# Performance work log

Measured on AMD Instinct MI355X. Metric: run time of the kernel, lower is better.

## Reference

```python
import jax, jax.numpy as jnp
import numpy as np

NEG = -1e15  # matches mask_logits constant -1000000000000000.0


def setup_inputs() -> dict:
    key = jax.random.key(0)
    ks = jax.random.split(key, 4)
    B, d, c_len, q_len = 64, 512, 1024, 128
    C = jax.random.normal(ks[0], (B, d, c_len), dtype=jnp.float32)
    Q = jax.random.normal(ks[1], (B, d, q_len), dtype=jnp.float32)
    c_mask = jnp.ones((B, c_len), dtype=jnp.float32)
    q_mask = jnp.ones((B, q_len), dtype=jnp.float32)
    W0 = jax.random.normal(ks[2], (3 * d,), dtype=jnp.float32) / np.sqrt(d).astype(np.float32)
    Wr = jax.random.normal(ks[3], (d, 4 * d), dtype=jnp.float32) * np.float32(0.02)
    return {"C": C, "Q": Q, "c_mask": c_mask, "q_mask": q_mask, "W0": W0, "Wr": Wr}


def reference(C, Q, c_mask, q_mask, W0, Wr):
    # C: [B, d, c], Q: [B, d, q]
    d = C.shape[1]
    C_t = jnp.swapaxes(C, 1, 2)  # [B, c, d]
    Q_t = jnp.swapaxes(Q, 1, 2)  # [B, q, d]
    w_c, w_q, w_m = W0[:d], W0[d:2 * d], W0[2 * d:]
    # Trilinear similarity, algebraically identical to cat([C,Q,C*Q]) @ W0
    S = (C_t @ w_c)[:, :, None] + (Q_t @ w_q)[:, None, :] \
        + jnp.einsum('bid,bjd->bij', C_t * w_m, Q_t)  # [B, c, q]
    qm = q_mask[:, None, :]  # [B, 1, q]
    cm = c_mask[:, :, None]  # [B, c, 1]
    S_bar = jax.nn.softmax(S * qm + NEG * (1.0 - qm), axis=2)
    S_bbar = jax.nn.softmax(S * cm + NEG * (1.0 - cm), axis=1)
    A = S_bar @ Q_t  # [B, c, d]
    Bm = jnp.einsum('bij,bkj->bik', S_bar, S_bbar) @ C_t  # [B, c, d]
    out = jnp.concatenate([C_t, A, C_t * A, C_t * Bm], axis=2)  # [B, c, 4d]
    # dropout inactive (eval mode); 1x1 conv == matmul with Wr [d, 4d]
    return jnp.einsum('od,bcd->boc', Wr, out)  # [B, d, c]
```

## Files before the change

kernel.cpp:

```cpp
#include <hip/hip_runtime.h>
#include <hip/hip_bf16.h>

typedef unsigned short u16;
typedef __attribute__((ext_vector_type(8))) short short8;
typedef __attribute__((ext_vector_type(4))) short short4v;
typedef __attribute__((ext_vector_type(4))) float f32x4;

#define NEGV -1000000000000000.0f
#define SBAR() asm volatile("s_barrier" ::: "memory")

__device__ __forceinline__ u16 f2bf(float f) {
  unsigned u = __float_as_uint(f);
  unsigned r = (u + 0x7FFFu + ((u >> 16) & 1u)) >> 16;
  return (u16)r;
}
__device__ __forceinline__ float bf2f(u16 s) {
  return __uint_as_float(((unsigned)s) << 16);
}
__device__ __forceinline__ void lds16(const void* g, void* l) {
  __builtin_amdgcn_global_load_lds((const __attribute__((address_space(1))) void*)g,
                                   (__attribute__((address_space(3))) void*)l,
                                   16, 0, 0);
}

__global__ __launch_bounds__(1024) void gemm8b(const u16* __restrict__ A,
                                               const u16* __restrict__ B,
                                               float* __restrict__ out) {
  extern __shared__ u16 lds[];
  const int bid = blockIdx.x;
  const int wg = (bid & 7) * 64 + (bid >> 3);
  const int m0 = (wg & 1) * 256;
  const int n0 = (wg >> 1) * 256;
  const int tid = threadIdx.x;
  const int lane = tid & 63;
  const int w = tid >> 6;
  const int wr = w >> 2;
  const int wc = w & 3;
  const int fro = lane & 15;
  const int hi = lane >> 4;
  const int kx = fro & 7;
  const int sr = lane >> 3;
  const int sgc = ((lane & 7) ^ sr) << 3;

  const u16* Ag = A + (size_t)m0 * 2048;
  const u16* Bg = B + (size_t)n0 * 2048;
  const int rA = wr * 64 + fro;
  const int rB = wc * 64 + fro;

  f32x4 acc[4][4] = {};

#define STG(gp, lp) \
  lds16((gp) + (size_t)(w * 8 + sr) * 2048 + sgc, (u16*)(lp) + w * 512)
#define RDF(base, row, k16) \
  (*(const short8*)&(base)[(size_t)(row) * 64 + (((k16) ^ kx) << 3)])

  STG(Ag, lds);
  STG(Ag + 262144, lds + 8192);
  STG(Bg, lds + 32768);
  STG(Bg + 262144, lds + 32768 + 8192);
  STG(Bg + 64, lds + 49152);
  STG(Bg + 262144 + 64, lds + 49152 + 8192);
  asm volatile("s_waitcnt vmcnt(2)" ::: "memory");
  SBAR();

  const u16* Ac = lds;
  u16* An = lds + 16384;
  const u16* Bc = lds + 32768;
  const u16* Bn = lds + 49152;
  u16* Bs2 = lds + 65536;

  for (int t = 0; t < 32; ++t) {
    const int kkA = (t < 31 ? t + 1 : 31) * 64;
    const int kkB = (t < 30 ? t + 2 : 31) * 64;
    short8 af[4], bf[4];

#pragma unroll
    for (int i = 0; i < 4; ++i) af[i] = RDF(Ac, rA + i * 16, hi);
#pragma unroll
    for (int j = 0; j < 4; ++j) bf[j] = RDF(Bc, rB + j * 16, hi);
    STG(Ag + kkA, An);
    STG(Ag + 262144 + kkA, An + 8192);
    SBAR();
    __builtin_amdgcn_s_setprio(1);
#pragma unroll
    for (int i = 0; i < 4; ++i)
#pragma unroll
      for (int j = 0; j < 4; ++j)
        acc[i][j] =
            __builtin_amdgcn_mfma_f32_16x16x32_bf16(af[i], bf[j], acc[i][j], 0, 0, 0);
    __builtin_amdgcn_s_setprio(0);
    SBAR();

#pragma unroll
    for (int i = 0; i < 4; ++i) af[i] = RDF(Ac, rA + i * 16, 4 + hi);
#pragma unroll
    for (int j = 0; j < 4; ++j) bf[j] = RDF(Bc, rB + j * 16, 4 + hi);
    STG(Bg + kkB, Bs2);
    STG(Bg + 262144 + kkB, Bs2 + 8192);
    asm volatile("s_waitcnt vmcnt(2)" ::: "memory");
    SBAR();
    __builtin_amdgcn_s_setprio(1);
#pragma unroll
    for (int i = 0; i < 4; ++i)
#pragma unroll
      for (int j = 0; j < 4; ++j)
        acc[i][j] =
            __builtin_amdgcn_mfma_f32_16x16x32_bf16(af[i], bf[j], acc[i][j], 0, 0, 0);
    __builtin_amdgcn_s_setprio(0);
    SBAR();

    u16* tA = An; An = (u16*)Ac; Ac = tA;
    u16* tB = (u16*)Bc; Bc = Bn; Bn = Bs2; Bs2 = tB;
  }
  asm volatile("s_waitcnt vmcnt(0)" ::: "memory");

  const int crow = m0 + wr * 64 + hi * 4;
#pragma unroll
  for (int i = 0; i < 4; ++i)
#pragma unroll
    for (int j = 0; j < 4; ++j) {
      const int n = n0 + wc * 64 + j * 16 + fro;
      float* op = out + (size_t)(n >> 10) * 524288 + (n & 1023);
#pragma unroll
      for (int g = 0; g < 4; ++g)
        op[(size_t)(crow + i * 16 + g) * 1024] = acc[i][j][g];
    }
#undef STG
#undef RDF
}

__global__ __launch_bounds__(256) void gemm_t(const u16* __restrict__ A,
                                              const u16* __restrict__ B,
                                              const float* __restrict__ csum,
                                              u16* __restrict__ Tt) {
  __shared__ u16 As[128 * 64];
  __shared__ u16 Bs[128 * 64];
  const int b = blockIdx.z;
  const int n0 = blockIdx.y * 128;
  const u16* Ab = A + (size_t)b * 131072;
  const u16* Bb = B + (size_t)b * 524288;
  const int t = threadIdx.x;
  const int lane = t & 63;
  const int w = t >> 6;
  const int wr = w >> 1, wc = w & 1;
  const int srow = lane >> 3;
  const int scol = (lane & 7) * 8;

  f32x4 acc[4][4] = {};

  for (int k0 = 0; k0 < 1024; k0 += 64) {
    __syncthreads();
#pragma unroll
    for (int qq = 0; qq < 4; ++qq) {
      const int q = w * 4 + qq;
      const int r = q * 8 + srow;
      lds16(Ab + (size_t)r * 1024 + k0 + scol, &As[q * 512]);
      lds16(Bb + (size_t)(n0 + r) * 1024 + k0 + scol, &Bs[q * 512]);
    }
    __syncthreads();
#pragma unroll
    for (int ks = 0; ks < 2; ++ks) {
      short8 af[4], bg[4];
      const int fro = lane & 15;
      const int k8 = ks * 32 + (lane >> 4) * 8;
#pragma unroll
      for (int i = 0; i < 4; ++i)
        af[i] = *(const short8*)&As[(wr * 64 + i * 16 + fro) * 64 + k8];
#pragma unroll
      for (int i = 0; i < 4; ++i)
        bg[i] = *(const short8*)&Bs[(wc * 64 + i * 16 + fro) * 64 + k8];
#pragma unroll
      for (int i = 0; i < 4; ++i)
#pragma unroll
        for (int j = 0; j < 4; ++j)
          acc[i][j] =
              __builtin_amdgcn_mfma_f32_16x16x32_bf16(af[i], bg[j], acc[i][j], 0, 0, 0);
    }
  }

  const int col = lane & 15;
  const int r4 = (lane >> 4) * 4;
#pragma unroll
  for (int i = 0; i < 4; ++i)
#pragma unroll
    for (int g = 0; g < 4; ++g) {
      const int rr = wr * 64 + i * 16 + r4 + g;
      const float inv = 1.f / csum[b * 128 + rr];
#pragma unroll
      for (int j = 0; j < 4; ++j) {
        const int cc = n0 + wc * 64 + j * 16 + col;
        Tt[(size_t)b * 65536 + (size_t)cc * 128 + rr] = f2bf(acc[i][j][g] * inv);
      }
    }
}

__global__ __launch_bounds__(256) void gemm_s(
    const u16* __restrict__ A, const u16* __restrict__ Bq,
    const float* __restrict__ cb, const float* __restrict__ qb,
    const float* __restrict__ cmask, const float* __restrict__ qmask,
    u16* __restrict__ Sbar, u16* __restrict__ EunT, float* __restrict__ csum) {
  __shared__ u16 As[128 * 64];
  __shared__ u16 Bs[128 * 64];
  __shared__ u16 Lt[128][136];
  __shared__ float rmaxs[2][128];
  __shared__ float rsums[2][128];
  __shared__ float cparts[2][128];
  const int b = blockIdx.z;
  const int m0 = blockIdx.x * 128;
  const u16* Ab = A + (size_t)b * 2097152;
  const u16* Bb = Bq + (size_t)b * 65536;
  const int t = threadIdx.x;
  const int lane = t & 63;
  const int w = t >> 6;
  const int wr = w >> 1, wc = w & 1;
  const int srow = lane >> 3;
  const int scol = (lane & 7) * 8;

  f32x4 acc[4][4] = {};

  for (int k0 = 0; k0 < 512; k0 += 64) {
    __syncthreads();
#pragma unroll
    for (int qq = 0; qq < 4; ++qq) {
      const int q = w * 4 + qq;
      const int r = q * 8 + srow;
      lds16(Ab + (size_t)(m0 + r) * 2048 + k0 + scol, &As[q * 512]);
      lds16(Bb + (size_t)r * 512 + k0 + scol, &Bs[q * 512]);
    }
    __syncthreads();
#pragma unroll
    for (int ks = 0; ks < 2; ++ks) {
      short8 af[4], bg[4];
      const int fro = lane & 15;
      const int k8 = ks * 32 + (lane >> 4) * 8;
#pragma unroll
      for (int i = 0; i < 4; ++i)
        af[i] = *(const short8*)&As[(wr * 64 + i * 16 + fro) * 64 + k8];
#pragma unroll
      for (int i = 0; i < 4; ++i)
        bg[i] = *(const short8*)&Bs[(wc * 64 + i * 16 + fro) * 64 + k8];
#pragma unroll
      for (int i = 0; i < 4; ++i)
#pragma unroll
        for (int j = 0; j < 4; ++j)
          acc[i][j] =
              __builtin_amdgcn_mfma_f32_16x16x32_bf16(af[i], bg[j], acc[i][j], 0, 0, 0);
    }
  }

  const int fro = lane & 15;
  const int hi = lane >> 4;
  float qv[4], qbv[4];
#pragma unroll
  for (int j = 0; j < 4; ++j) {
    const int cc = wc * 64 + j * 16 + fro;
    qv[j] = qmask[b * 128 + cc];
    qbv[j] = qb[b * 128 + cc];
  }
  float colp[4] = {0.f, 0.f, 0.f, 0.f};
#pragma unroll
  for (int i = 0; i < 4; ++i)
#pragma unroll
    for (int g = 0; g < 4; ++g) {
      const int rl = wr * 64 + i * 16 + hi * 4 + g;
      const float rb = cb[b * 1024 + m0 + rl];
      const float cv = cmask[b * 1024 + m0 + rl];
      const float coff = NEGV * (1.f - cv);
#pragma unroll
      for (int j = 0; j < 4; ++j) {
        const float v = acc[i][j][g] + rb + qbv[j];
        acc[i][j][g] = v;
        const float e = __expf(v * cv + coff);
        Lt[wc * 64 + j * 16 + fro][rl] = f2bf(e);
        colp[j] += e;
      }
    }
#pragma unroll
  for (int j = 0; j < 4; ++j) {
    colp[j] += __shfl_xor(colp[j], 16);
    colp[j] += __shfl_xor(colp[j], 32);
  }
  if (hi == 0)
#pragma unroll
    for (int j = 0; j < 4; ++j) cparts[wr][wc * 64 + j * 16 + fro] = colp[j];
  float rtmp[4][4];
#pragma unroll
  for (int i = 0; i < 4; ++i)
#pragma unroll
    for (int g = 0; g < 4; ++g) {
      float m = -3.4e38f;
#pragma unroll
      for (int j = 0; j < 4; ++j) {
        const float xm = acc[i][j][g] * qv[j] + NEGV * (1.f - qv[j]);
        acc[i][j][g] = xm;
        m = fmaxf(m, xm);
      }
#pragma unroll
      for (int o = 8; o; o >>= 1) m = fmaxf(m, __shfl_xor(m, o));
      rtmp[i][g] = m;
    }
  if (fro == 0)
#pragma unroll
    for (int i = 0; i < 4; ++i)
#pragma unroll
      for (int g = 0; g < 4; ++g)
        rmaxs[wc][wr * 64 + i * 16 + hi * 4 + g] = rtmp[i][g];
  __syncthreads();
  if (t < 128) atomicAdd(&csum[b * 128 + t], cparts[0][t] + cparts[1][t]);
  {
    const int jr = t >> 1;
    const int ih = (t & 1) * 64;
    u16* dst = EunT + (size_t)b * 131072 + (size_t)jr * 1024 + m0 + ih;
#pragma unroll
    for (int s = 0; s < 8; ++s)
      *(short8*)(dst + s * 8) = *(const short8*)&Lt[jr][ih + s * 8];
  }
#pragma unroll
  for (int i = 0; i < 4; ++i)
#pragma unroll
    for (int g = 0; g < 4; ++g) {
      const int rl = wr * 64 + i * 16 + hi * 4 + g;
      const float M = fmaxf(rmaxs[0][rl], rmaxs[1][rl]);
      float s = 0.f;
#pragma unroll
      for (int j = 0; j < 4; ++j) {
        const float p = __expf(acc[i][j][g] - M);
        acc[i][j][g] = p;
        s += p;
      }
#pragma unroll
      for (int o = 8; o; o >>= 1) s += __shfl_xor(s, o);
      rtmp[i][g] = s;
    }
  if (fro == 0)
#pragma unroll
    for (int i = 0; i < 4; ++i)
#pragma unroll
      for (int g = 0; g < 4; ++g)
        rsums[wc][wr * 64 + i * 16 + hi * 4 + g] = rtmp[i][g];
  __syncthreads();
#pragma unroll
  for (int i = 0; i < 4; ++i)
#pragma unroll
    for (int g = 0; g < 4; ++g) {
      const int rl = wr * 64 + i * 16 + hi * 4 + g;
      const float inv = 1.f / (rsums[0][rl] + rsums[1][rl]);
#pragma unroll
      for (int j = 0; j < 4; ++j)
        Sbar[((size_t)b * 1024 + m0 + rl) * 128 + wc * 64 + j * 16 + fro] =
            f2bf(acc[i][j][g] * inv);
    }
}

__global__ __launch_bounds__(512) void gemm_ab2(const u16* __restrict__ Sbar,
                                                const u16* __restrict__ Qo,
                                                const u16* __restrict__ Tt,
                                                u16* __restrict__ O) {
  extern __shared__ u16 sh[];
  u16* LQ = sh;
  u16* LT = sh + 16384;
  u16* Ls = sh + 65536;
  const int dcol = blockIdx.x * 128;
  const int b = blockIdx.y;
  const int t = threadIdx.x;
  const int lane = t & 63;
  const int w = t >> 6;
  const int wr = w >> 2, wc = w & 3;
  const int fro = lane & 15, hi = lane >> 4;
  const int srow4 = t >> 4;
  const int sslot = t & 15;

  const u16* Qg = Qo + (size_t)b * 65536 + (size_t)dcol * 128;
  const u16* Tg = Tt + (size_t)b * 65536 + (size_t)dcol * 128;
  const u16* Sg = Sbar + (size_t)b * 131072;

#define STG32(gp, lp)                                                         \
  {                                                                           \
    _Pragma("unroll") for (int ii = 0; ii < 4; ++ii) {                        \
      const int row_ = ii * 32 + srow4;                                       \
      lds16((gp) + (size_t)row_ * 128 + ((sslot ^ (row_ & 7)) << 3),          \
            (u16*)(lp) + ii * 4096 + t * 8);                                  \
    }                                                                         \
  }
#define RDS(base, row, kslot)                                                 \
  (*(const short8*)&(base)[(size_t)(row) * 128 + (((kslot) ^ ((row) & 7)) << 3)])

  STG32(Qg, LQ);
  STG32(Tg, LT);
  STG32(Sg, sh + 32768);
  asm volatile("s_waitcnt vmcnt(0)" ::: "memory");
  __syncthreads();

  for (int mm = 0; mm < 8; ++mm) {
    const u16* LSc = sh + 32768 + ((size_t)(mm & 1) << 14);
    u16* LSn = sh + 32768 + ((size_t)((mm + 1) & 1) << 14);
    if (mm < 7) STG32(Sg + (size_t)(mm + 1) * 16384, LSn);

    f32x4 aa[4][2] = {};
    f32x4 ab[4][2] = {};
#pragma unroll
    for (int ks = 0; ks < 4; ++ks) {
      short8 af[4], bq[2], bt[2];
#pragma unroll
      for (int i = 0; i < 4; ++i) {
        const int r = wr * 64 + i * 16 + fro;
        af[i] = RDS(LSc, r, ks * 4 + hi);
      }
#pragma unroll
      for (int j = 0; j < 2; ++j) {
        const int r = wc * 32 + j * 16 + fro;
        bq[j] = RDS(LQ, r, ks * 4 + hi);
        bt[j] = RDS(LT, r, ks * 4 + hi);
      }
#pragma unroll
      for (int i = 0; i < 4; ++i)
#pragma unroll
        for (int j = 0; j < 2; ++j) {
          aa[i][j] =
              __builtin_amdgcn_mfma_f32_16x16x32_bf16(af[i], bq[j], aa[i][j], 0, 0, 0);
          ab[i][j] =
              __builtin_amdgcn_mfma_f32_16x16x32_bf16(af[i], bt[j], ab[i][j], 0, 0, 0);
        }
    }

    const size_t obase = (size_t)b * 2097152 + (size_t)mm * 262144 + dcol;
    __syncthreads();
#pragma unroll
    for (int i = 0; i < 4; ++i)
#pragma unroll
      for (int j = 0; j < 2; ++j)
#pragma unroll
        for (int g = 0; g < 4; ++g)
          Ls[(wr * 64 + i * 16 + hi * 4 + g) * 128 + wc * 32 + j * 16 + fro] =
              f2bf(aa[i][j][g]);
    __syncthreads();
    short8 c8[4];
#pragma unroll
    for (int it = 0; it < 4; ++it) {
      const int row = it * 32 + srow4;
      const short8 a8 = *(const short8*)&Ls[row * 128 + sslot * 8];
      c8[it] = *(const short8*)&O[obase + (size_t)row * 2048 + sslot * 8];
      short8 p2;
#pragma unroll
      for (int k = 0; k < 8; ++k)
        p2[k] = (short)f2bf(bf2f((u16)c8[it][k]) * bf2f((u16)a8[k]));
      *(short8*)&O[obase + (size_t)row * 2048 + sslot * 8 + 512] = a8;
      *(short8*)&O[obase + (size_t)row * 2048 + sslot * 8 + 1024] = p2;
    }
    __syncthreads();
#pragma unroll
    for (int i = 0; i < 4; ++i)
#pragma unroll
      for (int j = 0; j < 2; ++j)
#pragma unroll
        for (int g = 0; g < 4; ++g)
          Ls[(wr * 64 + i * 16 + hi * 4 + g) * 128 + wc * 32 + j * 16 + fro] =
              f2bf(ab[i][j][g]);
    __syncthreads();
#pragma unroll
    for (int it = 0; it < 4; ++it) {
      const int row = it * 32 + srow4;
      const short8 b8 = *(const short8*)&Ls[row * 128 + sslot * 8];
      short8 p3;
#pragma unroll
      for (int k = 0; k < 8; ++k)
        p3[k] = (short)f2bf(bf2f((u16)c8[it][k]) * bf2f((u16)b8[k]));
      *(short8*)&O[obase + (size_t)row * 2048 + sslot * 8 + 1536] = p3;
    }
    __syncthreads();
  }
#undef STG32
#undef RDS
}

__global__ __launch_bounds__(256) void prep_C(const float* __restrict__ C,
                                              const float* __restrict__ W0,
                                              u16* __restrict__ O,
                                              u16* __restrict__ Corig,
                                              float* __restrict__ cb) {
  __shared__ float L[64][65];
  __shared__ float P[4][64];
  const int b = blockIdx.z;
  const int d0 = blockIdx.y * 64;
  const int i0 = blockIdx.x * 64;
  const int t = threadIdx.x;
  const int cx = t & 63;
  const int rb = t >> 6;
  const float* Cb = C + ((size_t)b * 512 + d0) * 1024 + i0;
  float part = 0.f;
#pragma unroll
  for (int rr = 0; rr < 16; ++rr) {
    const int r = rb * 16 + rr;
    const float v = Cb[(size_t)r * 1024 + cx];
    L[r][cx] = v;
    part = fmaf(v, W0[d0 + r], part);
    Corig[((size_t)b * 512 + d0 + r) * 1024 + i0 + cx] = f2bf(v);
  }
  P[rb][cx] = part;
  __syncthreads();
#pragma unroll
  for (int rr = 0; rr < 16; ++rr) {
    const int il = rb * 16 + rr;
    O[((size_t)b * 1024 + i0 + il) * 2048 + d0 + cx] = f2bf(L[cx][il]);
  }
  if (rb == 0)
    atomicAdd(&cb[b * 1024 + i0 + cx], P[0][cx] + P[1][cx] + P[2][cx] + P[3][cx]);
}

__global__ __launch_bounds__(256) void prep_Q(const float* __restrict__ Q,
                                              const float* __restrict__ W0,
                                              u16* __restrict__ Qmb,
                                              u16* __restrict__ Qorig,
                                              float* __restrict__ qb) {
  __shared__ float L[64][65];
  __shared__ float P[4][64];
  const int b = blockIdx.z;
  const int d0 = blockIdx.y * 64;
  const int j0 = blockIdx.x * 64;
  const int t = threadIdx.x;
  const int cx = t & 63;
  const int rb = t >> 6;
  const float* Qb = Q + ((size_t)b * 512 + d0) * 128 + j0;
  float part = 0.f;
#pragma unroll
  for (int rr = 0; rr < 16; ++rr) {
    const int r = rb * 16 + rr;
    const float v = Qb[(size_t)r * 128 + cx];
    L[r][cx] = v;
    part = fmaf(v, W0[512 + d0 + r], part);
    Qorig[((size_t)b * 512 + d0 + r) * 128 + j0 + cx] = f2bf(v);
  }
  P[rb][cx] = part;
  __syncthreads();
  const float wm = W0[1024 + d0 + cx];
#pragma unroll
  for (int rr = 0; rr < 16; ++rr) {
    const int jl = rb * 16 + rr;
    Qmb[((size_t)b * 128 + j0 + jl) * 512 + d0 + cx] = f2bf(L[cx][jl] * wm);
  }
  if (rb == 0)
    atomicAdd(&qb[b * 128 + j0 + cx], P[0][cx] + P[1][cx] + P[2][cx] + P[3][cx]);
}

__global__ __launch_bounds__(256) void cvt_wr(const float* __restrict__ Wr,
                                              u16* __restrict__ Wrb) {
  const int idx = blockIdx.x * 256 + threadIdx.x;
  const float4 v = ((const float4*)Wr)[idx];
  short4v o;
  o[0] = (short)f2bf(v.x);
  o[1] = (short)f2bf(v.y);
  o[2] = (short)f2bf(v.z);
  o[3] = (short)f2bf(v.w);
  *(short4v*)&Wrb[(size_t)idx * 4] = o;
}

extern "C" void kernel_launch(void* const* d_in, const int* in_sizes, int n_in,
                              void* d_out, int out_size, void* d_ws, size_t ws_size,
                              hipStream_t stream) {
  (void)in_sizes; (void)n_in; (void)out_size;
  const float* C = (const float*)d_in[0];
  const float* Q = (const float*)d_in[1];
  const float* cm = (const float*)d_in[2];
  const float* qm = (const float*)d_in[3];
  const float* W0 = (const float*)d_in[4];
  const float* Wr = (const float*)d_in[5];
  float* out = (float*)d_out;

  if (ws_size < 405078016ull) return;

  char* p = (char*)d_ws;
  u16* O     = (u16*)(p);
  u16* Corig = (u16*)(p + 268435456ull);
  u16* Qmb   = (u16*)(p + 335544320ull);
  u16* Qorig = (u16*)(p + 343932928ull);
  u16* EunT  = (u16*)(p + 360710144ull);
  u16* Sbar  = (u16*)(p + 377487360ull);
  u16* Tt    = (u16*)(p + 394264576ull);
  u16* Wrb   = (u16*)(p + 402653184ull);
  float* cb  = (float*)(p + 404750336ull);
  float* qb  = (float*)(p + 405012480ull);
  float* csum= (float*)(p + 405045248ull);

  (void)hipFuncSetAttribute((const void*)gemm8b,
                            hipFuncAttributeMaxDynamicSharedMemorySize, 163840);
  (void)hipFuncSetAttribute((const void*)gemm_ab2,
                            hipFuncAttributeMaxDynamicSharedMemorySize, 163840);
  (void)hipMemsetAsync(cb, 0, 327680, stream);

  cvt_wr<<<dim3(1024), dim3(256), 0, stream>>>(Wr, Wrb);
  prep_C<<<dim3(16, 8, 64), dim3(256), 0, stream>>>(C, W0, O, Corig, cb);
  prep_Q<<<dim3(2, 8, 64), dim3(256), 0, stream>>>(Q, W0, Qmb, Qorig, qb);

  gemm_s<<<dim3(8, 1, 64), dim3(256), 0, stream>>>(O, Qmb, cb, qb, cm, qm,
                                                   Sbar, EunT, csum);

  gemm_t<<<dim3(1, 4, 64), dim3(256), 0, stream>>>(EunT, Corig, csum, Tt);

  gemm_ab2<<<dim3(4, 64), dim3(512), 163840, stream>>>(Sbar, Qorig, Tt, O);

  gemm8b<<<dim3(512), dim3(1024), 163840, stream>>>(Wrb, O, out);
}
```

Before: 355.7 us.

## Fuse attention-output GEMMs with final projection to drop the concat buffer

Replaces the separate gemm_ab2 and gemm8b kernels with one fused kernel, gemm_f. For each 128-row context tile it computes S_bar·Q, S_bar·T and the elementwise products with C in LDS, then multiplies each 128-wide chunk directly by the matching slice of Wr. This removes the large [B, c, 4d] bf16 intermediate, which was written to and read back from global memory. prep_C and gemm_s now use a compact 512-stride C^T buffer, and the workspace shrinks. The cost is that every block re-streams all of Wr through LDS with no double-buffering and many barriers, and the 160KB LDS footprint limits occupancy to one block per CU. The tuned pipelined projection GEMM is lost as well.

```diff
diff --git a/kernel.cpp b/kernel.cpp
--- a/kernel.cpp
+++ b/kernel.cpp
@@ -7,7 +7,6 @@
 typedef __attribute__((ext_vector_type(4))) float f32x4;
 
 #define NEGV -1000000000000000.0f
-#define SBAR() asm volatile("s_barrier" ::: "memory")
 
 __device__ __forceinline__ u16 f2bf(float f) {
   unsigned u = __float_as_uint(f);
@@ -23,110 +22,155 @@
                                    16, 0, 0);
 }
 
-__global__ __launch_bounds__(1024) void gemm8b(const u16* __restrict__ A,
-                                               const u16* __restrict__ B,
-                                               float* __restrict__ out) {
-  extern __shared__ u16 lds[];
-  const int bid = blockIdx.x;
-  const int wg = (bid & 7) * 64 + (bid >> 3);
-  const int m0 = (wg & 1) * 256;
-  const int n0 = (wg >> 1) * 256;
-  const int tid = threadIdx.x;
-  const int lane = tid & 63;
-  const int w = tid >> 6;
-  const int wr = w >> 2;
-  const int wc = w & 3;
-  const int fro = lane & 15;
-  const int hi = lane >> 4;
-  const int kx = fro & 7;
-  const int sr = lane >> 3;
-  const int sgc = ((lane & 7) ^ sr) << 3;
-
-  const u16* Ag = A + (size_t)m0 * 2048;
-  const u16* Bg = B + (size_t)n0 * 2048;
-  const int rA = wr * 64 + fro;
-  const int rB = wc * 64 + fro;
-
-  f32x4 acc[4][4] = {};
-
-#define STG(gp, lp) \
-  lds16((gp) + (size_t)(w * 8 + sr) * 2048 + sgc, (u16*)(lp) + w * 512)
-#define RDF(base, row, k16) \
-  (*(const short8*)&(base)[(size_t)(row) * 64 + (((k16) ^ kx) << 3)])
-
-  STG(Ag, lds);
-  STG(Ag + 262144, lds + 8192);
-  STG(Bg, lds + 32768);
-  STG(Bg + 262144, lds + 32768 + 8192);
-  STG(Bg + 64, lds + 49152);
-  STG(Bg + 262144 + 64, lds + 49152 + 8192);
-  asm volatile("s_waitcnt vmcnt(2)" ::: "memory");
-  SBAR();
-
-  const u16* Ac = lds;
-  u16* An = lds + 16384;
-  const u16* Bc = lds + 32768;
-  const u16* Bn = lds + 49152;
-  u16* Bs2 = lds + 65536;
-
-  for (int t = 0; t < 32; ++t) {
-    const int kkA = (t < 31 ? t + 1 : 31) * 64;
-    const int kkB = (t < 30 ? t + 2 : 31) * 64;
-    short8 af[4], bf[4];
-
-#pragma unroll
-    for (int i = 0; i < 4; ++i) af[i] = RDF(Ac, rA + i * 16, hi);
-#pragma unroll
-    for (int j = 0; j < 4; ++j) bf[j] = RDF(Bc, rB + j * 16, hi);
-    STG(Ag + kkA, An);
-    STG(Ag + 262144 + kkA, An + 8192);
-    SBAR();
-    __builtin_amdgcn_s_setprio(1);
+__global__ __launch_bounds__(512, 2) void gemm_f(
+    const u16* __restrict__ Sb, const u16* __restrict__ Qo,
+    const u16* __restrict__ Tt, const u16* __restrict__ Ct,
+    const u16* __restrict__ Wrb, float* __restrict__ out) {
+  extern __shared__ u16 sh[];
+  u16* S  = sh;
+  u16* R1 = sh + 16384;
+  u16* R2 = sh + 32768;
+  u16* R3 = sh + 49152;
+  u16* R4 = sh + 65536;
+  const int mt = blockIdx.x;
+  const int b  = blockIdx.y;
+  const int m0 = mt * 128;
+  const int t = threadIdx.x;
+  const int lane = t & 63;
+  const int w = t >> 6;
+  const int fro = lane & 15, hi = lane >> 4;
+  const int srow4 = t >> 4;
+  const int sslot = t & 15;
+  const int o1 = (w >> 1) * 64;
+  const int cb2 = (w & 1) * 64;
+
+#define STG32(gp, ld, lp)                                                     \
+  {                                                                           \
+    _Pragma("unroll") for (int ii = 0; ii < 4; ++ii) {                        \
+      const int row_ = ii * 32 + srow4;                                       \
+      lds16((gp) + (size_t)row_ * (ld) + ((sslot ^ (row_ & 7)) << 3),         \
+            (u16*)(lp) + ii * 4096 + t * 8);                                  \
+    }                                                                         \
+  }
+#define RDS(base, row, kslot)                                                 \
+  (*(const short8*)&(base)[(size_t)(row) * 128 + (((kslot) ^ ((row) & 7)) << 3)])
+
+  f32x4 OA[2][4][4] = {};
+
+  STG32(Sb + (size_t)b * 131072 + (size_t)m0 * 128, 128, S);
+  __syncthreads();
+
+  for (int dcol = 0; dcol < 4; ++dcol) {
+    STG32(Qo + (size_t)b * 65536 + (size_t)(dcol * 128) * 128, 128, R1);
+    STG32(Tt + (size_t)b * 65536 + (size_t)(dcol * 128) * 128, 128, R2);
+    STG32(Ct + (size_t)b * 524288 + (size_t)m0 * 512 + dcol * 128, 512, R4);
+    __syncthreads();
+
+    {
+      f32x4 p[8] = {};
+#pragma unroll
+      for (int ks = 0; ks < 4; ++ks) {
+        const short8 af = RDS(S, w * 16 + fro, ks * 4 + hi);
+        short8 bf[8];
+#pragma unroll
+        for (int jd = 0; jd < 8; ++jd) bf[jd] = RDS(R2, jd * 16 + fro, ks * 4 + hi);
+#pragma unroll
+        for (int jd = 0; jd < 8; ++jd)
+          p[jd] = __builtin_amdgcn_mfma_f32_16x16x32_bf16(af, bf[jd], p[jd], 0, 0, 0);
+      }
+#pragma unroll
+      for (int jd = 0; jd < 8; ++jd)
+#pragma unroll
+        for (int g = 0; g < 4; ++g) {
+          const int c = w * 16 + hi * 4 + g;
+          const int d = jd * 16 + fro;
+          const int a = c * 128 + (((d >> 3) ^ (c & 7)) << 3) + (d & 7);
+          R3[a] = f2bf(p[jd][g] * bf2f(R4[a]));
+        }
+    }
+    f32x4 paa[8] = {};
+#pragma unroll
+    for (int ks = 0; ks < 4; ++ks) {
+      const short8 af = RDS(S, w * 16 + fro, ks * 4 + hi);
+      short8 bf[8];
+#pragma unroll
+      for (int jd = 0; jd < 8; ++jd) bf[jd] = RDS(R1, jd * 16 + fro, ks * 4 + hi);
+#pragma unroll
+      for (int jd = 0; jd < 8; ++jd)
+        paa[jd] = __builtin_amdgcn_mfma_f32_16x16x32_bf16(af, bf[jd], paa[jd], 0, 0, 0);
+    }
+    __syncthreads();
+
+#pragma unroll
+    for (int cc = 0; cc < 4; ++cc) {
+      const int ch = (cc == 0) ? 3 : cc - 1;
+      if (ch == 1 || ch == 2) {
+#pragma unroll
+        for (int jd = 0; jd < 8; ++jd)
+#pragma unroll
+          for (int g = 0; g < 4; ++g) {
+            const int c = w * 16 + hi * 4 + g;
+            const int d = jd * 16 + fro;
+            const int a = c * 128 + (((d >> 3) ^ (c & 7)) << 3) + (d & 7);
+            R3[a] = f2bf(ch == 1 ? paa[jd][g] : paa[jd][g] * bf2f(R4[a]));
+          }
+      }
+      const u16* Wp = Wrb + (size_t)ch * 512 + (size_t)dcol * 128;
+      STG32(Wp, 2048, R1);
+      STG32(Wp + (size_t)128 * 2048, 2048, R2);
+      __syncthreads();
+      const u16* Bp = (ch == 0) ? R4 : R3;
+#pragma unroll
+      for (int ks = 0; ks < 4; ++ks) {
+        short8 af[4], bfr[4];
+#pragma unroll
+        for (int i = 0; i < 4; ++i) af[i] = RDS(R1, o1 + i * 16 + fro, ks * 4 + hi);
+#pragma unroll
+        for (int j = 0; j < 4; ++j) bfr[j] = RDS(Bp, cb2 + j * 16 + fro, ks * 4 + hi);
+#pragma unroll
+        for (int i = 0; i < 4; ++i)
+#pragma unroll
+          for (int j = 0; j < 4; ++j)
+            OA[0][i][j] = __builtin_amdgcn_mfma_f32_16x16x32_bf16(
+                af[i], bfr[j], OA[0][i][j], 0, 0, 0);
+      }
+      __syncthreads();
+      STG32(Wp + (size_t)256 * 2048, 2048, R1);
+      STG32(Wp + (size_t)384 * 2048, 2048, R2);
+      __syncthreads();
+#pragma unroll
+      for (int ks = 0; ks < 4; ++ks) {
+        short8 af[4], bfr[4];
+#pragma unroll
+        for (int i = 0; i < 4; ++i) af[i] = RDS(R1, o1 + i * 16 + fro, ks * 4 + hi);
+#pragma unroll
+        for (int j = 0; j < 4; ++j) bfr[j] = RDS(Bp, cb2 + j * 16 + fro, ks * 4 + hi);
+#pragma unroll
+        for (int i = 0; i < 4; ++i)
+#pragma unroll
+          for (int j = 0; j < 4; ++j)
+            OA[1][i][j] = __builtin_amdgcn_mfma_f32_16x16x32_bf16(
+                af[i], bfr[j], OA[1][i][j], 0, 0, 0);
+      }
+      __syncthreads();
+    }
+  }
+
+  float* ob = out + (size_t)b * 524288;
+#pragma unroll
+  for (int oh = 0; oh < 2; ++oh)
 #pragma unroll
     for (int i = 0; i < 4; ++i)
 #pragma unroll
-      for (int j = 0; j < 4; ++j)
-        acc[i][j] =
-            __builtin_amdgcn_mfma_f32_16x16x32_bf16(af[i], bf[j], acc[i][j], 0, 0, 0);
-    __builtin_amdgcn_s_setprio(0);
-    SBAR();
-
-#pragma unroll
-    for (int i = 0; i < 4; ++i) af[i] = RDF(Ac, rA + i * 16, 4 + hi);
-#pragma unroll
-    for (int j = 0; j < 4; ++j) bf[j] = RDF(Bc, rB + j * 16, 4 + hi);
-    STG(Bg + kkB, Bs2);
-    STG(Bg + 262144 + kkB, Bs2 + 8192);
-    asm volatile("s_waitcnt vmcnt(2)" ::: "memory");
-    SBAR();
-    __builtin_amdgcn_s_setprio(1);
-#pragma unroll
-    for (int i = 0; i < 4; ++i)
-#pragma unroll
-      for (int j = 0; j < 4; ++j)
-        acc[i][j] =
-            __builtin_amdgcn_mfma_f32_16x16x32_bf16(af[i], bf[j], acc[i][j], 0, 0, 0);
-    __builtin_amdgcn_s_setprio(0);
-    SBAR();
-
-    u16* tA = An; An = (u16*)Ac; Ac = tA;
-    u16* tB = (u16*)Bc; Bc = Bn; Bn = Bs2; Bs2 = tB;
-  }
-  asm volatile("s_waitcnt vmcnt(0)" ::: "memory");
-
-  const int crow = m0 + wr * 64 + hi * 4;
-#pragma unroll
-  for (int i = 0; i < 4; ++i)
-#pragma unroll
-    for (int j = 0; j < 4; ++j) {
-      const int n = n0 + wc * 64 + j * 16 + fro;
-      float* op = out + (size_t)(n >> 10) * 524288 + (n & 1023);
-#pragma unroll
-      for (int g = 0; g < 4; ++g)
-        op[(size_t)(crow + i * 16 + g) * 1024] = acc[i][j][g];
-    }
-#undef STG
-#undef RDF
+      for (int j = 0; j < 4; ++j) {
+        const int o = oh * 256 + o1 + i * 16 + hi * 4;
+        const int c = m0 + cb2 + j * 16 + fro;
+#pragma unroll
+        for (int g = 0; g < 4; ++g)
+          ob[(size_t)(o + g) * 1024 + c] = OA[oh][i][j][g];
+      }
+#undef STG32
+#undef RDS
 }
 
 __global__ __launch_bounds__(256) void gemm_t(const u16* __restrict__ A,
@@ -207,7 +251,7 @@
   __shared__ float cparts[2][128];
   const int b = blockIdx.z;
   const int m0 = blockIdx.x * 128;
-  const u16* Ab = A + (size_t)b * 2097152;
+  const u16* Ab = A + (size_t)b * 524288;
   const u16* Bb = Bq + (size_t)b * 65536;
   const int t = threadIdx.x;
   const int lane = t & 63;
@@ -224,7 +268,7 @@
     for (int qq = 0; qq < 4; ++qq) {
       const int q = w * 4 + qq;
       const int r = q * 8 + srow;
-      lds16(Ab + (size_t)(m0 + r) * 2048 + k0 + scol, &As[q * 512]);
+      lds16(Ab + (size_t)(m0 + r) * 512 + k0 + scol, &As[q * 512]);
       lds16(Bb + (size_t)r * 512 + k0 + scol, &Bs[q * 512]);
     }
     __syncthreads();
@@ -352,130 +396,9 @@
     }
 }
 
-__global__ __launch_bounds__(512) void gemm_ab2(const u16* __restrict__ Sbar,
-                                                const u16* __restrict__ Qo,
-                                                const u16* __restrict__ Tt,
-                                                u16* __restrict__ O) {
-  extern __shared__ u16 sh[];
-  u16* LQ = sh;
-  u16* LT = sh + 16384;
-  u16* Ls = sh + 65536;
-  const int dcol = blockIdx.x * 128;
-  const int b = blockIdx.y;
-  const int t = threadIdx.x;
-  const int lane = t & 63;
-  const int w = t >> 6;
-  const int wr = w >> 2, wc = w & 3;
-  const int fro = lane & 15, hi = lane >> 4;
-  const int srow4 = t >> 4;
-  const int sslot = t & 15;
-
-  const u16* Qg = Qo + (size_t)b * 65536 + (size_t)dcol * 128;
-  const u16* Tg = Tt + (size_t)b * 65536 + (size_t)dcol * 128;
-  const u16* Sg = Sbar + (size_t)b * 131072;
-
-#define STG32(gp, lp)                                                         \
-  {                                                                           \
-    _Pragma("unroll") for (int ii = 0; ii < 4; ++ii) {                        \
-      const int row_ = ii * 32 + srow4;                                       \
-      lds16((gp) + (size_t)row_ * 128 + ((sslot ^ (row_ & 7)) << 3),          \
-            (u16*)(lp) + ii * 4096 + t * 8);                                  \
-    }                                                                         \
-  }
-#define RDS(base, row, kslot)                                                 \
-  (*(const short8*)&(base)[(size_t)(row) * 128 + (((kslot) ^ ((row) & 7)) << 3)])
-
-  STG32(Qg, LQ);
-  STG32(Tg, LT);
-  STG32(Sg, sh + 32768);
-  asm volatile("s_waitcnt vmcnt(0)" ::: "memory");
-  __syncthreads();
-
-  for (int mm = 0; mm < 8; ++mm) {
-    const u16* LSc = sh + 32768 + ((size_t)(mm & 1) << 14);
-    u16* LSn = sh + 32768 + ((size_t)((mm + 1) & 1) << 14);
-    if (mm < 7) STG32(Sg + (size_t)(mm + 1) * 16384, LSn);
-
-    f32x4 aa[4][2] = {};
-    f32x4 ab[4][2] = {};
-#pragma unroll
-    for (int ks = 0; ks < 4; ++ks) {
-      short8 af[4], bq[2], bt[2];
-#pragma unroll
-      for (int i = 0; i < 4; ++i) {
-        const int r = wr * 64 + i * 16 + fro;
-        af[i] = RDS(LSc, r, ks * 4 + hi);
-      }
-#pragma unroll
-      for (int j = 0; j < 2; ++j) {
-        const int r = wc * 32 + j * 16 + fro;
-        bq[j] = RDS(LQ, r, ks * 4 + hi);
-        bt[j] = RDS(LT, r, ks * 4 + hi);
-      }
-#pragma unroll
-      for (int i = 0; i < 4; ++i)
-#pragma unroll
-        for (int j = 0; j < 2; ++j) {
-          aa[i][j] =
-              __builtin_amdgcn_mfma_f32_16x16x32_bf16(af[i], bq[j], aa[i][j], 0, 0, 0);
-          ab[i][j] =
-              __builtin_amdgcn_mfma_f32_16x16x32_bf16(af[i], bt[j], ab[i][j], 0, 0, 0);
-        }
-    }
-
-    const size_t obase = (size_t)b * 2097152 + (size_t)mm * 262144 + dcol;
-    __syncthreads();
-#pragma unroll
-    for (int i = 0; i < 4; ++i)
-#pragma unroll
-      for (int j = 0; j < 2; ++j)
-#pragma unroll
-        for (int g = 0; g < 4; ++g)
-          Ls[(wr * 64 + i * 16 + hi * 4 + g) * 128 + wc * 32 + j * 16 + fro] =
-              f2bf(aa[i][j][g]);
-    __syncthreads();
-    short8 c8[4];
-#pragma unroll
-    for (int it = 0; it < 4; ++it) {
-      const int row = it * 32 + srow4;
-      const short8 a8 = *(const short8*)&Ls[row * 128 + sslot * 8];
-      c8[it] = *(const short8*)&O[obase + (size_t)row * 2048 + sslot * 8];
-      short8 p2;
-#pragma unroll
-      for (int k = 0; k < 8; ++k)
-        p2[k] = (short)f2bf(bf2f((u16)c8[it][k]) * bf2f((u16)a8[k]));
-      *(short8*)&O[obase + (size_t)row * 2048 + sslot * 8 + 512] = a8;
-      *(short8*)&O[obase + (size_t)row * 2048 + sslot * 8 + 1024] = p2;
-    }
-    __syncthreads();
-#pragma unroll
-    for (int i = 0; i < 4; ++i)
-#pragma unroll
-      for (int j = 0; j < 2; ++j)
-#pragma unroll
-        for (int g = 0; g < 4; ++g)
-          Ls[(wr * 64 + i * 16 + hi * 4 + g) * 128 + wc * 32 + j * 16 + fro] =
-              f2bf(ab[i][j][g]);
-    __syncthreads();
-#pragma unroll
-    for (int it = 0; it < 4; ++it) {
-      const int row = it * 32 + srow4;
-      const short8 b8 = *(const short8*)&Ls[row * 128 + sslot * 8];
-      short8 p3;
-#pragma unroll
-      for (int k = 0; k < 8; ++k)
-        p3[k] = (short)f2bf(bf2f((u16)c8[it][k]) * bf2f((u16)b8[k]));
-      *(short8*)&O[obase + (size_t)row * 2048 + sslot * 8 + 1536] = p3;
-    }
-    __syncthreads();
-  }
-#undef STG32
-#undef RDS
-}
-
 __global__ __launch_bounds__(256) void prep_C(const float* __restrict__ C,
                                               const float* __restrict__ W0,
-                                              u16* __restrict__ O,
+                                              u16* __restrict__ Ct,
                                               u16* __restrict__ Corig,
                                               float* __restrict__ cb) {
   __shared__ float L[64][65];
@@ -501,7 +424,7 @@
 #pragma unroll
   for (int rr = 0; rr < 16; ++rr) {
     const int il = rb * 16 + rr;
-    O[((size_t)b * 1024 + i0 + il) * 2048 + d0 + cx] = f2bf(L[cx][il]);
+    Ct[((size_t)b * 1024 + i0 + il) * 512 + d0 + cx] = f2bf(L[cx][il]);
   }
   if (rb == 0)
     atomicAdd(&cb[b * 1024 + i0 + cx], P[0][cx] + P[1][cx] + P[2][cx] + P[3][cx]);
@@ -566,37 +489,34 @@
   const float* Wr = (const float*)d_in[5];
   float* out = (float*)d_out;
 
-  if (ws_size < 405078016ull) return;
+  if (ws_size < 195362816ull) return;
 
   char* p = (char*)d_ws;
-  u16* O     = (u16*)(p);
-  u16* Corig = (u16*)(p + 268435456ull);
-  u16* Qmb   = (u16*)(p + 335544320ull);
-  u16* Qorig = (u16*)(p + 343932928ull);
-  u16* EunT  = (u16*)(p + 360710144ull);
-  u16* Sbar  = (u16*)(p + 377487360ull);
-  u16* Tt    = (u16*)(p + 394264576ull);
-  u16* Wrb   = (u16*)(p + 402653184ull);
-  float* cb  = (float*)(p + 404750336ull);
-  float* qb  = (float*)(p + 405012480ull);
-  float* csum= (float*)(p + 405045248ull);
-
-  (void)hipFuncSetAttribute((const void*)gemm8b,
-                            hipFuncAttributeMaxDynamicSharedMemorySize, 163840);
-  (void)hipFuncSetAttribute((const void*)gemm_ab2,
+  u16* Ct    = (u16*)(p);
+  u16* Corig = (u16*)(p + 67108864ull);
+  u16* Qmb   = (u16*)(p + 134217728ull);
+  u16* Qorig = (u16*)(p + 142606336ull);
+  u16* EunT  = (u16*)(p + 150994944ull);
+  u16* Sbar  = (u16*)(p + 167772160ull);
+  u16* Tt    = (u16*)(p + 184549376ull);
+  u16* Wrb   = (u16*)(p + 192937984ull);
+  float* cb  = (float*)(p + 195035136ull);
+  float* qb  = (float*)(p + 195297280ull);
+  float* csum= (float*)(p + 195330048ull);
+
+  (void)hipFuncSetAttribute((const void*)gemm_f,
                             hipFuncAttributeMaxDynamicSharedMemorySize, 163840);
   (void)hipMemsetAsync(cb, 0, 327680, stream);
 
   cvt_wr<<<dim3(1024), dim3(256), 0, stream>>>(Wr, Wrb);
-  prep_C<<<dim3(16, 8, 64), dim3(256), 0, stream>>>(C, W0, O, Corig, cb);
+  prep_C<<<dim3(16, 8, 64), dim3(256), 0, stream>>>(C, W0, Ct, Corig, cb);
   prep_Q<<<dim3(2, 8, 64), dim3(256), 0, stream>>>(Q, W0, Qmb, Qorig, qb);
 
-  gemm_s<<<dim3(8, 1, 64), dim3(256), 0, stream>>>(O, Qmb, cb, qb, cm, qm,
+  gemm_s<<<dim3(8, 1, 64), dim3(256), 0, stream>>>(Ct, Qmb, cb, qb, cm, qm,
                                                    Sbar, EunT, csum);
 
   gemm_t<<<dim3(1, 4, 64), dim3(256), 0, stream>>>(EunT, Corig, csum, Tt);
 
-  gemm_ab2<<<dim3(4, 64), dim3(512), 163840, stream>>>(Sbar, Qorig, Tt, O);
-
-  gemm8b<<<dim3(512), dim3(1024), 163840, stream>>>(Wrb, O, out);
-}
+  gemm_f<<<dim3(8, 64), dim3(512), 163840, stream>>>(Sbar, Qorig, Tt, Ct, Wrb,
+                                                     out);
+}
```

After: 546.4 us. 1.54x slower.

## Fuse T-matrix GEMM into the attention-apply kernel, dropping the Tt round trip

Applied to the files above, without the earlier changes.

Removes the separate gemm_t launch and computes T = EunT·Corig^T (scaled by the column softmax sums) inside the gemm_tab kernel, writing it straight into shared memory in the swizzled layout that the following stage reads. This drops a kernel launch and the global write and re-read of the Tt intermediate. In exchange, each 512-thread block runs a simple unpipelined K loop over 1024 with two barriers per step before its main work starts, and the grid is unchanged (4x64 blocks), so the serial prologue could lengthen the kernel. The STG offset edit in gemm8b computes the same address and has no effect.

```diff
diff --git a/kernel.cpp b/kernel.cpp
--- a/kernel.cpp
+++ b/kernel.cpp
@@ -59,7 +59,7 @@
   STG(Bg, lds + 32768);
   STG(Bg + 262144, lds + 32768 + 8192);
   STG(Bg + 64, lds + 49152);
-  STG(Bg + 262144 + 64, lds + 49152 + 8192);
+  STG(Bg + 262144 + 64, lds + 57344);
   asm volatile("s_waitcnt vmcnt(2)" ::: "memory");
   SBAR();
 
@@ -127,71 +127,6 @@
     }
 #undef STG
 #undef RDF
-}
-
-__global__ __launch_bounds__(256) void gemm_t(const u16* __restrict__ A,
-                                              const u16* __restrict__ B,
-                                              const float* __restrict__ csum,
-                                              u16* __restrict__ Tt) {
-  __shared__ u16 As[128 * 64];
-  __shared__ u16 Bs[128 * 64];
-  const int b = blockIdx.z;
-  const int n0 = blockIdx.y * 128;
-  const u16* Ab = A + (size_t)b * 131072;
-  const u16* Bb = B + (size_t)b * 524288;
-  const int t = threadIdx.x;
-  const int lane = t & 63;
-  const int w = t >> 6;
-  const int wr = w >> 1, wc = w & 1;
-  const int srow = lane >> 3;
-  const int scol = (lane & 7) * 8;
-
-  f32x4 acc[4][4] = {};
-
-  for (int k0 = 0; k0 < 1024; k0 += 64) {
-    __syncthreads();
-#pragma unroll
-    for (int qq = 0; qq < 4; ++qq) {
-      const int q = w * 4 + qq;
-      const int r = q * 8 + srow;
-      lds16(Ab + (size_t)r * 1024 + k0 + scol, &As[q * 512]);
-      lds16(Bb + (size_t)(n0 + r) * 1024 + k0 + scol, &Bs[q * 512]);
-    }
-    __syncthreads();
-#pragma unroll
-    for (int ks = 0; ks < 2; ++ks) {
-      short8 af[4], bg[4];
-      const int fro = lane & 15;
-      const int k8 = ks * 32 + (lane >> 4) * 8;
-#pragma unroll
-      for (int i = 0; i < 4; ++i)
-        af[i] = *(const short8*)&As[(wr * 64 + i * 16 + fro) * 64 + k8];
-#pragma unroll
-      for (int i = 0; i < 4; ++i)
-        bg[i] = *(const short8*)&Bs[(wc * 64 + i * 16 + fro) * 64 + k8];
-#pragma unroll
-      for (int i = 0; i < 4; ++i)
-#pragma unroll
-        for (int j = 0; j < 4; ++j)
-          acc[i][j] =
-              __builtin_amdgcn_mfma_f32_16x16x32_bf16(af[i], bg[j], acc[i][j], 0, 0, 0);
-    }
-  }
-
-  const int col = lane & 15;
-  const int r4 = (lane >> 4) * 4;
-#pragma unroll
-  for (int i = 0; i < 4; ++i)
-#pragma unroll
-    for (int g = 0; g < 4; ++g) {
-      const int rr = wr * 64 + i * 16 + r4 + g;
-      const float inv = 1.f / csum[b * 128 + rr];
-#pragma unroll
-      for (int j = 0; j < 4; ++j) {
-        const int cc = n0 + wc * 64 + j * 16 + col;
-        Tt[(size_t)b * 65536 + (size_t)cc * 128 + rr] = f2bf(acc[i][j][g] * inv);
-      }
-    }
 }
 
 __global__ __launch_bounds__(256) void gemm_s(
@@ -352,13 +287,15 @@
     }
 }
 
-__global__ __launch_bounds__(512) void gemm_ab2(const u16* __restrict__ Sbar,
-                                                const u16* __restrict__ Qo,
-                                                const u16* __restrict__ Tt,
-                                                u16* __restrict__ O) {
+__global__ __launch_bounds__(512) void gemm_tab(
+    const u16* __restrict__ EunT, const u16* __restrict__ Corig,
+    const float* __restrict__ csum, const u16* __restrict__ Sbar,
+    const u16* __restrict__ Qo, u16* __restrict__ O) {
   extern __shared__ u16 sh[];
   u16* LQ = sh;
   u16* LT = sh + 16384;
+  u16* TA = sh + 32768;
+  u16* TB = sh + 40960;
   u16* Ls = sh + 65536;
   const int dcol = blockIdx.x * 128;
   const int b = blockIdx.y;
@@ -370,10 +307,6 @@
   const int srow4 = t >> 4;
   const int sslot = t & 15;
 
-  const u16* Qg = Qo + (size_t)b * 65536 + (size_t)dcol * 128;
-  const u16* Tg = Tt + (size_t)b * 65536 + (size_t)dcol * 128;
-  const u16* Sg = Sbar + (size_t)b * 131072;
-
 #define STG32(gp, lp)                                                         \
   {                                                                           \
     _Pragma("unroll") for (int ii = 0; ii < 4; ++ii) {                        \
@@ -384,9 +317,63 @@
   }
 #define RDS(base, row, kslot)                                                 \
   (*(const short8*)&(base)[(size_t)(row) * 128 + (((kslot) ^ ((row) & 7)) << 3)])
-
-  STG32(Qg, LQ);
-  STG32(Tg, LT);
+#define TSTG(gp, lp)                                                          \
+  {                                                                           \
+    _Pragma("unroll") for (int q = 0; q < 2; ++q) {                           \
+      const int row_ = q * 64 + (t >> 3);                                     \
+      lds16((gp) + (size_t)row_ * 1024 + ((t & 7) << 3),                      \
+            (u16*)(lp) + q * 4096 + t * 8);                                   \
+    }                                                                         \
+  }
+
+  STG32(Qo + (size_t)b * 65536 + (size_t)dcol * 128, LQ);
+
+  {
+    const u16* Ag = EunT + (size_t)b * 131072;
+    const u16* Bg = Corig + (size_t)b * 524288 + (size_t)dcol * 1024;
+    f32x4 acc[4][2] = {};
+    for (int k0 = 0; k0 < 1024; k0 += 64) {
+      __syncthreads();
+      TSTG(Ag + k0, TA);
+      TSTG(Bg + k0, TB);
+      __syncthreads();
+#pragma unroll
+      for (int ks = 0; ks < 2; ++ks) {
+        short8 af[4], bg[2];
+        const int k8 = ks * 32 + hi * 8;
+#pragma unroll
+        for (int i = 0; i < 4; ++i)
+          af[i] = *(const short8*)&TA[(wr * 64 + i * 16 + fro) * 64 + k8];
+#pragma unroll
+        for (int jf = 0; jf < 2; ++jf)
+          bg[jf] = *(const short8*)&TB[(wc * 32 + jf * 16 + fro) * 64 + k8];
+#pragma unroll
+        for (int i = 0; i < 4; ++i)
+#pragma unroll
+          for (int jf = 0; jf < 2; ++jf)
+            acc[i][jf] = __builtin_amdgcn_mfma_f32_16x16x32_bf16(
+                af[i], bg[jf], acc[i][jf], 0, 0, 0);
+      }
+    }
+    const int col = lane & 15;
+    const int r4 = hi * 4;
+#pragma unroll
+    for (int i = 0; i < 4; ++i)
+#pragma unroll
+      for (int g = 0; g < 4; ++g) {
+        const int j = wr * 64 + i * 16 + r4 + g;
+        const float inv = 1.f / csum[b * 128 + j];
+#pragma unroll
+        for (int jf = 0; jf < 2; ++jf) {
+          const int d = wc * 32 + jf * 16 + col;
+          LT[d * 128 + (((j >> 3) ^ (d & 7)) << 3) + (j & 7)] =
+              f2bf(acc[i][jf][g] * inv);
+        }
+      }
+  }
+  __syncthreads();
+
+  const u16* Sg = Sbar + (size_t)b * 131072;
   STG32(Sg, sh + 32768);
   asm volatile("s_waitcnt vmcnt(0)" ::: "memory");
   __syncthreads();
@@ -471,6 +458,7 @@
   }
 #undef STG32
 #undef RDS
+#undef TSTG
 }
 
 __global__ __launch_bounds__(256) void prep_C(const float* __restrict__ C,
@@ -575,7 +563,6 @@
   u16* Qorig = (u16*)(p + 343932928ull);
   u16* EunT  = (u16*)(p + 360710144ull);
   u16* Sbar  = (u16*)(p + 377487360ull);
-  u16* Tt    = (u16*)(p + 394264576ull);
   u16* Wrb   = (u16*)(p + 402653184ull);
   float* cb  = (float*)(p + 404750336ull);
   float* qb  = (float*)(p + 405012480ull);
@@ -583,7 +570,7 @@
 
   (void)hipFuncSetAttribute((const void*)gemm8b,
                             hipFuncAttributeMaxDynamicSharedMemorySize, 163840);
-  (void)hipFuncSetAttribute((const void*)gemm_ab2,
+  (void)hipFuncSetAttribute((const void*)gemm_tab,
                             hipFuncAttributeMaxDynamicSharedMemorySize, 163840);
   (void)hipMemsetAsync(cb, 0, 327680, stream);
 
@@ -594,9 +581,8 @@
   gemm_s<<<dim3(8, 1, 64), dim3(256), 0, stream>>>(O, Qmb, cb, qb, cm, qm,
                                                    Sbar, EunT, csum);
 
-  gemm_t<<<dim3(1, 4, 64), dim3(256), 0, stream>>>(EunT, Corig, csum, Tt);
-
-  gemm_ab2<<<dim3(4, 64), dim3(512), 163840, stream>>>(Sbar, Qorig, Tt, O);
+  gemm_tab<<<dim3(4, 64), dim3(512), 163840, stream>>>(EunT, Corig, csum,
+                                                       Sbar, Qorig, O);
 
   gemm8b<<<dim3(512), dim3(1024), 163840, stream>>>(Wrb, O, out);
 }
```

New measurement: 351.0 us. About the same (-1.3%).
